# Kernel tuning notes

Hardware: AMD Instinct MI355X
Metric: run time of the kernel (lower is better)

The kernel has to match this reference:

```python
import jax, jax.numpy as jnp
import numpy as np

B = 65536          # batch (number of states)
M = 32             # obstacles per state -> x width = 2*M
PHI = [4, 64, 64, 64]
RHO = [64, 64, 64, 32]


def _init_mlp(key, dims, prefix):
    params = {}
    ks = jax.random.split(key, len(dims) - 1)
    for i, (din, dout) in enumerate(zip(dims[:-1], dims[1:])):
        scale = 1.0 / np.sqrt(din)
        params[f"{prefix}_W{i+1}"] = scale * jax.random.normal(ks[i], (din, dout), dtype=jnp.float32)
        params[f"{prefix}_b{i+1}"] = jnp.zeros((dout,), dtype=jnp.float32)
    return params


def setup_inputs() -> dict:
    key = jax.random.key(0)
    kx, kv, kphi, krho = jax.random.split(key, 4)
    inp = {
        "x": jax.random.normal(kx, (B, 2 * M), dtype=jnp.float32),
        "vel": jax.random.normal(kv, (B, 2), dtype=jnp.float32),
    }
    inp.update(_init_mlp(kphi, PHI, "phi"))
    inp.update(_init_mlp(krho, RHO, "rho"))
    return inp


def _mlp3(h, W1, b1, W2, b2, W3, b3):
    # FeedForward: activation between hidden layers, linear output
    h = jax.nn.relu(h @ W1 + b1)
    h = jax.nn.relu(h @ W2 + b2)
    return h @ W3 + b3


def reference(x, vel,
              phi_W1, phi_b1, phi_W2, phi_b2, phi_W3, phi_b3,
              rho_W1, rho_b1, rho_W2, rho_b2, rho_W3, rho_b3):
    b = x.shape[0]
    m = x.shape[1] // 2
    obs = x.reshape(b, m, 2)                                   # [B, M, 2]
    velb = jnp.broadcast_to(vel[:, None, :], (b, m, 2))        # [B, M, 2]
    inp = jnp.concatenate([obs, velb], axis=-1)                # [B, M, 4]
    # phi batched across all obstacle elements (replaces the per-i loop)
    h = _mlp3(inp, phi_W1, phi_b1, phi_W2, phi_b2, phi_W3, phi_b3)  # [B, M, 64]
    X = h.sum(axis=1)                                          # DeepSets sum pool -> [B, 64]
    return _mlp3(X, rho_W1, rho_b1, rho_W2, rho_b2, rho_W3, rho_b3)  # [B, 32]
```

## Files before the change

kernel.cpp:

```cpp
#include <hip/hip_runtime.h>

typedef _Float16 h16x8 __attribute__((ext_vector_type(8)));
typedef _Float16 h16x4 __attribute__((ext_vector_type(4)));
typedef _Float16 h16x2 __attribute__((ext_vector_type(2)));
typedef float    fx4   __attribute__((ext_vector_type(4)));

static __device__ __forceinline__ fx4 mfma16(h16x8 a, h16x8 b, fx4 c) {
  return __builtin_amdgcn_mfma_f32_16x16x32_f16(a, b, c, 0, 0, 0);
}

static __device__ __forceinline__ h16x2 splat2(float v) {
  const _Float16 h = (_Float16)v;
  h16x2 r; r[0] = h; r[1] = h; return r;
}

union ABfrag { h16x2 p[4]; h16x8 v; };


__global__ __launch_bounds__(256, 2)
void deepset_kernel(const float* __restrict__ x,   const float* __restrict__ vel,
                    const float* __restrict__ pW1, const float* __restrict__ pb1,
                    const float* __restrict__ pW2, const float* __restrict__ pb2,
                    const float* __restrict__ pW3, const float* __restrict__ pb3,
                    const float* __restrict__ rW1, const float* __restrict__ rb1,
                    const float* __restrict__ rW2, const float* __restrict__ rb2,
                    const float* __restrict__ rW3, const float* __restrict__ rb3,
                    float* __restrict__ out)
{
  __shared__ __align__(16) _Float16 h2T[4][16][72];
  __shared__ __align__(16) _Float16 Xlds[4][16][72];

  const int tid  = threadIdx.x;
  const int wave = tid >> 6;
  const int lane = tid & 63;
  const int q    = lane >> 4;
  const int c    = lane & 15;

  h16x2 wx[2][4], wy[2][4], wvx[2][4], wvy[2][4], bbp[2][4];
#pragma unroll
  for (int ks = 0; ks < 2; ++ks)
#pragma unroll
    for (int t = 0; t < 4; ++t) {
      const int f0 = 32*ks + 8*q + 2*t;
#pragma unroll
      for (int e = 0; e < 2; ++e) {
        wx [ks][t][e] = (_Float16)pW1[      f0 + e];
        wy [ks][t][e] = (_Float16)pW1[ 64 + f0 + e];
        wvx[ks][t][e] = (_Float16)pW1[128 + f0 + e];
        wvy[ks][t][e] = (_Float16)pW1[192 + f0 + e];
        bbp[ks][t][e] = (_Float16)pb1[      f0 + e];
      }
    }

  h16x8 B2[4][2];
#pragma unroll
  for (int ct = 0; ct < 4; ++ct)
#pragma unroll
    for (int ks = 0; ks < 2; ++ks) {
      h16x8 f2;
#pragma unroll
      for (int j = 0; j < 8; ++j)
        f2[j] = (_Float16)pW2[(32*ks + 8*q + j)*64 + 16*ct + c];
      B2[ct][ks] = f2;
    }
  float b2v[4];
#pragma unroll
  for (int ct = 0; ct < 4; ++ct) b2v[ct] = pb2[16*ct + c];

  const int sBaseBlock = blockIdx.x * 64;
  const int sBase = sBaseBlock + wave * 16;
  const h16x2 z2 = splat2(0.f);

  float4 xo_cur = ((const float4*)x)[(size_t)sBase*16 + c];
  float2 v_cur  = *(const float2*)(vel + 2*(size_t)sBase);

#pragma unroll 1
  for (int si = 0; si < 16; ++si) {
    float4 xo_nxt;
    float2 v_nxt;
    if (si < 15) {
      xo_nxt = ((const float4*)x)[(size_t)(sBase + si + 1)*16 + c];
      v_nxt  = *(const float2*)(vel + 2*(size_t)(sBase + si + 1));
    }
    const h16x2 vxp = splat2(v_cur.x);
    const h16x2 vyp = splat2(v_cur.y);
    h16x2 vbp[2][4];
#pragma unroll
    for (int ks = 0; ks < 2; ++ks)
#pragma unroll
      for (int t = 0; t < 4; ++t)
        vbp[ks][t] = vxp * wvx[ks][t] + vyp * wvy[ks][t] + bbp[ks][t];

    float Xacc[4] = {0.f, 0.f, 0.f, 0.f};
#pragma unroll
    for (int hh = 0; hh < 2; ++hh) {
      const h16x2 oxp = splat2(hh ? xo_cur.z : xo_cur.x);
      const h16x2 oyp = splat2(hh ? xo_cur.w : xo_cur.y);
      h16x8 A1[2];
#pragma unroll
      for (int ks = 0; ks < 2; ++ks) {
        ABfrag a;
#pragma unroll
        for (int t = 0; t < 4; ++t) {
          const h16x2 h = oxp * wx[ks][t] + oyp * wy[ks][t] + vbp[ks][t];
          a.p[t] = __builtin_elementwise_max(h, z2);
        }
        A1[ks] = a.v;
      }
#pragma unroll
      for (int ct = 0; ct < 4; ++ct) {
        fx4 acc = {0.f, 0.f, 0.f, 0.f};
        acc = mfma16(A1[0], B2[ct][0], acc);
        acc = mfma16(A1[1], B2[ct][1], acc);
#pragma unroll
        for (int r = 0; r < 4; ++r)
          Xacc[ct] += fmaxf(acc[r] + b2v[ct], 0.f);
      }
    }
#pragma unroll
    for (int ct = 0; ct < 4; ++ct) {
      float v = Xacc[ct];
      v += __shfl_down(v, 16);
      v += __shfl_down(v, 32);
      if (lane < 16) Xlds[wave][si][16*ct + c] = (_Float16)v;
    }
    xo_cur = xo_nxt;
    v_cur  = v_nxt;
  }

  __builtin_amdgcn_s_waitcnt(0xC07F);
  __builtin_amdgcn_wave_barrier();

  h16x8 B3[4][2];
#pragma unroll
  for (int ct = 0; ct < 4; ++ct)
#pragma unroll
    for (int ks = 0; ks < 2; ++ks) {
      h16x8 f3;
#pragma unroll
      for (int j = 0; j < 8; ++j)
        f3[j] = (_Float16)pW3[(32*ks + 8*q + j)*64 + 16*ct + c];
      B3[ct][ks] = f3;
    }
  float b3s[4];
#pragma unroll
  for (int ct = 0; ct < 4; ++ct) b3s[ct] = 32.f * pb3[16*ct + c];

  h16x8 AX[2];
#pragma unroll
  for (int ks = 0; ks < 2; ++ks)
    AX[ks] = *(const h16x8*)&Xlds[wave][c][32*ks + 8*q];

  fx4 C3[4];
#pragma unroll
  for (int ct = 0; ct < 4; ++ct) {
    fx4 acc = {0.f,0.f,0.f,0.f};
    acc = mfma16(AX[0], B3[ct][0], acc);
    acc = mfma16(AX[1], B3[ct][1], acc);
    C3[ct] = acc;
  }
#pragma unroll
  for (int r = 0; r < 4; ++r) {
    h16x4 pk;
#pragma unroll
    for (int ct = 0; ct < 4; ++ct)
      pk[ct] = (_Float16)(C3[ct][r] + b3s[ct]);
    *(h16x4*)&h2T[wave][4*q + r][4*c] = pk;
  }

  h16x8 R1[4][2], R2[4][2], R3[2][2];
#pragma unroll
  for (int ct = 0; ct < 4; ++ct)
#pragma unroll
    for (int ks = 0; ks < 2; ++ks) {
      h16x8 f1, f2;
#pragma unroll
      for (int j = 0; j < 8; ++j) {
        const int p = 32*ks + 8*q + j;
        const int f = 16*(p & 3) + (p >> 2);
        f1[j] = (_Float16)rW1[f*64 + 16*ct + c];
        f2[j] = (_Float16)rW2[f*64 + 16*ct + c];
      }
      R1[ct][ks] = f1;
      R2[ct][ks] = f2;
    }
#pragma unroll
  for (int ct = 0; ct < 2; ++ct)
#pragma unroll
    for (int ks = 0; ks < 2; ++ks) {
      h16x8 f3;
#pragma unroll
      for (int j = 0; j < 8; ++j) {
        const int p = 32*ks + 8*q + j;
        const int f = 16*(p & 3) + (p >> 2);
        f3[j] = (_Float16)rW3[f*32 + 16*ct + c];
      }
      R3[ct][ks] = f3;
    }
  float rb1v[4], rb2v[4], rb3v[2];
#pragma unroll
  for (int ct = 0; ct < 4; ++ct) { rb1v[ct] = rb1[16*ct + c]; rb2v[ct] = rb2[16*ct + c]; }
#pragma unroll
  for (int ct = 0; ct < 2; ++ct) rb3v[ct] = rb3[16*ct + c];

  __builtin_amdgcn_s_waitcnt(0xC07F);
  __builtin_amdgcn_wave_barrier();
  h16x8 A1r[2];
#pragma unroll
  for (int ks = 0; ks < 2; ++ks)
    A1r[ks] = *(const h16x8*)&h2T[wave][c][32*ks + 8*q];
  __builtin_amdgcn_wave_barrier();

  fx4 D1[4];
#pragma unroll
  for (int ct = 0; ct < 4; ++ct) {
    fx4 acc = {0.f,0.f,0.f,0.f};
    acc = mfma16(A1r[0], R1[ct][0], acc);
    acc = mfma16(A1r[1], R1[ct][1], acc);
    D1[ct] = acc;
  }
#pragma unroll
  for (int r = 0; r < 4; ++r) {
    h16x4 pk;
#pragma unroll
    for (int ct = 0; ct < 4; ++ct)
      pk[ct] = (_Float16)fmaxf(D1[ct][r] + rb1v[ct], 0.f);
    *(h16x4*)&h2T[wave][4*q + r][4*c] = pk;
  }
  __builtin_amdgcn_s_waitcnt(0xC07F);
  __builtin_amdgcn_wave_barrier();
  h16x8 A2r[2];
#pragma unroll
  for (int ks = 0; ks < 2; ++ks)
    A2r[ks] = *(const h16x8*)&h2T[wave][c][32*ks + 8*q];
  __builtin_amdgcn_wave_barrier();

  fx4 D2[4];
#pragma unroll
  for (int ct = 0; ct < 4; ++ct) {
    fx4 acc = {0.f,0.f,0.f,0.f};
    acc = mfma16(A2r[0], R2[ct][0], acc);
    acc = mfma16(A2r[1], R2[ct][1], acc);
    D2[ct] = acc;
  }
#pragma unroll
  for (int r = 0; r < 4; ++r) {
    h16x4 pk;
#pragma unroll
    for (int ct = 0; ct < 4; ++ct)
      pk[ct] = (_Float16)fmaxf(D2[ct][r] + rb2v[ct], 0.f);
    *(h16x4*)&h2T[wave][4*q + r][4*c] = pk;
  }
  __builtin_amdgcn_s_waitcnt(0xC07F);
  __builtin_amdgcn_wave_barrier();
  h16x8 A3r[2];
#pragma unroll
  for (int ks = 0; ks < 2; ++ks)
    A3r[ks] = *(const h16x8*)&h2T[wave][c][32*ks + 8*q];
  __builtin_amdgcn_wave_barrier();

  fx4 D3[2];
#pragma unroll
  for (int ct = 0; ct < 2; ++ct) {
    fx4 acc = {0.f,0.f,0.f,0.f};
    acc = mfma16(A3r[0], R3[ct][0], acc);
    acc = mfma16(A3r[1], R3[ct][1], acc);
    D3[ct] = acc;
  }
  const int srow = sBaseBlock + 16*wave + 4*q;
#pragma unroll
  for (int ct = 0; ct < 2; ++ct)
#pragma unroll
    for (int r = 0; r < 4; ++r)
      out[(size_t)(srow + r)*32 + 16*ct + c] = D3[ct][r] + rb3v[ct];
}

extern "C" void kernel_launch(void* const* d_in, const int* in_sizes, int n_in,
                              void* d_out, int out_size, void* d_ws, size_t ws_size,
                              hipStream_t stream) {
  const float* x   = (const float*)d_in[0];
  const float* vel = (const float*)d_in[1];
  const float* pW1 = (const float*)d_in[2];
  const float* pb1 = (const float*)d_in[3];
  const float* pW2 = (const float*)d_in[4];
  const float* pb2 = (const float*)d_in[5];
  const float* pW3 = (const float*)d_in[6];
  const float* pb3 = (const float*)d_in[7];
  const float* rW1 = (const float*)d_in[8];
  const float* rb1 = (const float*)d_in[9];
  const float* rW2 = (const float*)d_in[10];
  const float* rb2 = (const float*)d_in[11];
  const float* rW3 = (const float*)d_in[12];
  const float* rb3 = (const float*)d_in[13];
  float* out = (float*)d_out;

  const int B = in_sizes[0] / 64;
  deepset_kernel<<<dim3(B / 64), dim3(256), 0, stream>>>(
      x, vel, pW1, pb1, pW2, pb2, pW3, pb3,
      rW1, rb1, rW2, rb2, rW3, rb3, out);
}
```

Before: 136.0 us.

## Prepack fp16 weight fragments in a prep kernel and use single-wave blocks of 8 states

```diff
diff --git a/kernel.cpp b/kernel.cpp
--- a/kernel.cpp
+++ b/kernel.cpp
@@ -8,77 +8,105 @@
 static __device__ __forceinline__ fx4 mfma16(h16x8 a, h16x8 b, fx4 c) {
   return __builtin_amdgcn_mfma_f32_16x16x32_f16(a, b, c, 0, 0, 0);
 }
-
 static __device__ __forceinline__ h16x2 splat2(float v) {
-  const _Float16 h = (_Float16)v;
-  h16x2 r; r[0] = h; r[1] = h; return r;
-}
-
+  const _Float16 h = (_Float16)v; h16x2 r; r[0] = h; r[1] = h; return r;
+}
 union ABfrag { h16x2 p[4]; h16x8 v; };
 
 
-__global__ __launch_bounds__(256, 2)
-void deepset_kernel(const float* __restrict__ x,   const float* __restrict__ vel,
-                    const float* __restrict__ pW1, const float* __restrict__ pb1,
-                    const float* __restrict__ pW2, const float* __restrict__ pb2,
-                    const float* __restrict__ pW3, const float* __restrict__ pb3,
-                    const float* __restrict__ rW1, const float* __restrict__ rb1,
-                    const float* __restrict__ rW2, const float* __restrict__ rb2,
-                    const float* __restrict__ rW3, const float* __restrict__ rb3,
-                    float* __restrict__ out)
+__global__ __launch_bounds__(64)
+void prep_weights(const float* __restrict__ pW1, const float* __restrict__ pb1,
+                  const float* __restrict__ pW2, const float* __restrict__ pb2,
+                  const float* __restrict__ pW3, const float* __restrict__ pb3,
+                  const float* __restrict__ rW1, const float* __restrict__ rb1,
+                  const float* __restrict__ rW2, const float* __restrict__ rb2,
+                  const float* __restrict__ rW3, const float* __restrict__ rb3,
+                  _Float16* __restrict__ ws)
 {
-  __shared__ __align__(16) _Float16 h2T[4][16][72];
-  __shared__ __align__(16) _Float16 Xlds[4][16][72];
-
-  const int tid  = threadIdx.x;
-  const int wave = tid >> 6;
-  const int lane = tid & 63;
+  const int lane = threadIdx.x;
+  const int q = lane >> 4, c = lane & 15;
+  _Float16* W = ws + (size_t)lane * 512;
+
+#pragma unroll
+  for (int ct = 0; ct < 4; ++ct)
+#pragma unroll
+    for (int ks = 0; ks < 2; ++ks)
+#pragma unroll
+      for (int j = 0; j < 8; ++j) {
+        const int p = 32*ks + 8*q + j;
+        const int f = 16*(p & 3) + (p >> 2);
+        W[      (ct*2 + ks)*8 + j] = (_Float16)pW2[p*64 + 16*ct + c];
+        W[ 64 + (ct*2 + ks)*8 + j] = (_Float16)pW3[p*64 + 16*ct + c];
+        W[128 + (ct*2 + ks)*8 + j] = (_Float16)rW1[f*64 + 16*ct + c];
+        W[192 + (ct*2 + ks)*8 + j] = (_Float16)rW2[f*64 + 16*ct + c];
+        if (ct < 2)
+          W[256 + (ct*2 + ks)*8 + j] = (_Float16)rW3[f*32 + 16*ct + c];
+      }
+#pragma unroll
+  for (int ks = 0; ks < 2; ++ks)
+#pragma unroll
+    for (int i = 0; i < 8; ++i) {
+      const int f = 32*ks + 8*q + i;
+      W[288 + ks*8 + i] = (_Float16)pW1[      f];
+      W[304 + ks*8 + i] = (_Float16)pW1[ 64 + f];
+      W[320 + ks*8 + i] = (_Float16)pW1[128 + f];
+      W[336 + ks*8 + i] = (_Float16)pW1[192 + f];
+      W[352 + ks*8 + i] = (_Float16)pb1[      f];
+    }
+  float* F = (float*)(ws + (size_t)lane * 512) + 184;
+#pragma unroll
+  for (int ct = 0; ct < 4; ++ct) {
+    F[     ct] = pb2[16*ct + c];
+    F[ 4 + ct] = 32.f * pb3[16*ct + c];
+    F[ 8 + ct] = rb1[16*ct + c];
+    F[12 + ct] = rb2[16*ct + c];
+  }
+#pragma unroll
+  for (int ct = 0; ct < 2; ++ct) F[16 + ct] = rb3[16*ct + c];
+}
+
+__global__ __launch_bounds__(64, 5)
+void deepset_main(const float* __restrict__ x, const float* __restrict__ vel,
+                  const _Float16* __restrict__ ws, float* __restrict__ out)
+{
+  __shared__ __align__(16) _Float16 h2T[16][72];
+  __shared__ __align__(16) _Float16 Xlds[16][72];
+
+  const int lane = threadIdx.x & 63;
   const int q    = lane >> 4;
   const int c    = lane & 15;
 
-  h16x2 wx[2][4], wy[2][4], wvx[2][4], wvy[2][4], bbp[2][4];
-#pragma unroll
-  for (int ks = 0; ks < 2; ++ks)
-#pragma unroll
-    for (int t = 0; t < 4; ++t) {
-      const int f0 = 32*ks + 8*q + 2*t;
-#pragma unroll
-      for (int e = 0; e < 2; ++e) {
-        wx [ks][t][e] = (_Float16)pW1[      f0 + e];
-        wy [ks][t][e] = (_Float16)pW1[ 64 + f0 + e];
-        wvx[ks][t][e] = (_Float16)pW1[128 + f0 + e];
-        wvy[ks][t][e] = (_Float16)pW1[192 + f0 + e];
-        bbp[ks][t][e] = (_Float16)pb1[      f0 + e];
-      }
-    }
+  const h16x8* V = (const h16x8*)(ws + (size_t)lane * 512);
+  const float* F = (const float*)(ws + (size_t)lane * 512) + 184;
 
   h16x8 B2[4][2];
 #pragma unroll
   for (int ct = 0; ct < 4; ++ct)
 #pragma unroll
-    for (int ks = 0; ks < 2; ++ks) {
-      h16x8 f2;
-#pragma unroll
-      for (int j = 0; j < 8; ++j)
-        f2[j] = (_Float16)pW2[(32*ks + 8*q + j)*64 + 16*ct + c];
-      B2[ct][ks] = f2;
-    }
+    for (int ks = 0; ks < 2; ++ks) B2[ct][ks] = V[ct*2 + ks];
+  ABfrag wx[2], wy[2], wvx[2], wvy[2], bbp[2];
+#pragma unroll
+  for (int ks = 0; ks < 2; ++ks) {
+    wx [ks].v = V[36 + ks];
+    wy [ks].v = V[38 + ks];
+    wvx[ks].v = V[40 + ks];
+    wvy[ks].v = V[42 + ks];
+    bbp[ks].v = V[44 + ks];
+  }
   float b2v[4];
 #pragma unroll
-  for (int ct = 0; ct < 4; ++ct) b2v[ct] = pb2[16*ct + c];
-
-  const int sBaseBlock = blockIdx.x * 64;
-  const int sBase = sBaseBlock + wave * 16;
+  for (int ct = 0; ct < 4; ++ct) b2v[ct] = F[ct];
+
+  const int sBase = blockIdx.x * 8;
   const h16x2 z2 = splat2(0.f);
 
   float4 xo_cur = ((const float4*)x)[(size_t)sBase*16 + c];
   float2 v_cur  = *(const float2*)(vel + 2*(size_t)sBase);
 
 #pragma unroll 1
-  for (int si = 0; si < 16; ++si) {
-    float4 xo_nxt;
-    float2 v_nxt;
-    if (si < 15) {
+  for (int si = 0; si < 8; ++si) {
+    float4 xo_nxt; float2 v_nxt;
+    if (si < 7) {
       xo_nxt = ((const float4*)x)[(size_t)(sBase + si + 1)*16 + c];
       v_nxt  = *(const float2*)(vel + 2*(size_t)(sBase + si + 1));
     }
@@ -89,7 +117,7 @@
     for (int ks = 0; ks < 2; ++ks)
 #pragma unroll
       for (int t = 0; t < 4; ++t)
-        vbp[ks][t] = vxp * wvx[ks][t] + vyp * wvy[ks][t] + bbp[ks][t];
+        vbp[ks][t] = vxp * wvx[ks].p[t] + vyp * wvy[ks].p[t] + bbp[ks].p[t];
 
     float Xacc[4] = {0.f, 0.f, 0.f, 0.f};
 #pragma unroll
@@ -102,7 +130,7 @@
         ABfrag a;
 #pragma unroll
         for (int t = 0; t < 4; ++t) {
-          const h16x2 h = oxp * wx[ks][t] + oyp * wy[ks][t] + vbp[ks][t];
+          const h16x2 h = oxp * wx[ks].p[t] + oyp * wy[ks].p[t] + vbp[ks][t];
           a.p[t] = __builtin_elementwise_max(h, z2);
         }
         A1[ks] = a.v;
@@ -122,7 +150,7 @@
       float v = Xacc[ct];
       v += __shfl_down(v, 16);
       v += __shfl_down(v, 32);
-      if (lane < 16) Xlds[wave][si][16*ct + c] = (_Float16)v;
+      if (lane < 16) Xlds[si][16*ct + c] = (_Float16)v;
     }
     xo_cur = xo_nxt;
     v_cur  = v_nxt;
@@ -131,25 +159,33 @@
   __builtin_amdgcn_s_waitcnt(0xC07F);
   __builtin_amdgcn_wave_barrier();
 
-  h16x8 B3[4][2];
+  h16x8 B3[4][2], R1[4][2], R2[4][2], R3[2][2];
 #pragma unroll
   for (int ct = 0; ct < 4; ++ct)
 #pragma unroll
     for (int ks = 0; ks < 2; ++ks) {
-      h16x8 f3;
-#pragma unroll
-      for (int j = 0; j < 8; ++j)
-        f3[j] = (_Float16)pW3[(32*ks + 8*q + j)*64 + 16*ct + c];
-      B3[ct][ks] = f3;
-    }
-  float b3s[4];
-#pragma unroll
-  for (int ct = 0; ct < 4; ++ct) b3s[ct] = 32.f * pb3[16*ct + c];
+      B3[ct][ks] = V[ 8 + ct*2 + ks];
+      R1[ct][ks] = V[16 + ct*2 + ks];
+      R2[ct][ks] = V[24 + ct*2 + ks];
+    }
+#pragma unroll
+  for (int ct = 0; ct < 2; ++ct)
+#pragma unroll
+    for (int ks = 0; ks < 2; ++ks) R3[ct][ks] = V[32 + ct*2 + ks];
+  float b3s[4], rb1v[4], rb2v[4], rb3v[2];
+#pragma unroll
+  for (int ct = 0; ct < 4; ++ct) {
+    b3s[ct]  = F[ 4 + ct];
+    rb1v[ct] = F[ 8 + ct];
+    rb2v[ct] = F[12 + ct];
+  }
+#pragma unroll
+  for (int ct = 0; ct < 2; ++ct) rb3v[ct] = F[16 + ct];
 
   h16x8 AX[2];
 #pragma unroll
   for (int ks = 0; ks < 2; ++ks)
-    AX[ks] = *(const h16x8*)&Xlds[wave][c][32*ks + 8*q];
+    AX[ks] = *(const h16x8*)&Xlds[c][32*ks + 8*q];
 
   fx4 C3[4];
 #pragma unroll
@@ -165,50 +201,14 @@
 #pragma unroll
     for (int ct = 0; ct < 4; ++ct)
       pk[ct] = (_Float16)(C3[ct][r] + b3s[ct]);
-    *(h16x4*)&h2T[wave][4*q + r][4*c] = pk;
-  }
-
-  h16x8 R1[4][2], R2[4][2], R3[2][2];
-#pragma unroll
-  for (int ct = 0; ct < 4; ++ct)
-#pragma unroll
-    for (int ks = 0; ks < 2; ++ks) {
-      h16x8 f1, f2;
-#pragma unroll
-      for (int j = 0; j < 8; ++j) {
-        const int p = 32*ks + 8*q + j;
-        const int f = 16*(p & 3) + (p >> 2);
-        f1[j] = (_Float16)rW1[f*64 + 16*ct + c];
-        f2[j] = (_Float16)rW2[f*64 + 16*ct + c];
-      }
-      R1[ct][ks] = f1;
-      R2[ct][ks] = f2;
-    }
-#pragma unroll
-  for (int ct = 0; ct < 2; ++ct)
-#pragma unroll
-    for (int ks = 0; ks < 2; ++ks) {
-      h16x8 f3;
-#pragma unroll
-      for (int j = 0; j < 8; ++j) {
-        const int p = 32*ks + 8*q + j;
-        const int f = 16*(p & 3) + (p >> 2);
-        f3[j] = (_Float16)rW3[f*32 + 16*ct + c];
-      }
-      R3[ct][ks] = f3;
-    }
-  float rb1v[4], rb2v[4], rb3v[2];
-#pragma unroll
-  for (int ct = 0; ct < 4; ++ct) { rb1v[ct] = rb1[16*ct + c]; rb2v[ct] = rb2[16*ct + c]; }
-#pragma unroll
-  for (int ct = 0; ct < 2; ++ct) rb3v[ct] = rb3[16*ct + c];
-
+    *(h16x4*)&h2T[4*q + r][4*c] = pk;
+  }
   __builtin_amdgcn_s_waitcnt(0xC07F);
   __builtin_amdgcn_wave_barrier();
   h16x8 A1r[2];
 #pragma unroll
   for (int ks = 0; ks < 2; ++ks)
-    A1r[ks] = *(const h16x8*)&h2T[wave][c][32*ks + 8*q];
+    A1r[ks] = *(const h16x8*)&h2T[c][32*ks + 8*q];
   __builtin_amdgcn_wave_barrier();
 
   fx4 D1[4];
@@ -225,14 +225,14 @@
 #pragma unroll
     for (int ct = 0; ct < 4; ++ct)
       pk[ct] = (_Float16)fmaxf(D1[ct][r] + rb1v[ct], 0.f);
-    *(h16x4*)&h2T[wave][4*q + r][4*c] = pk;
+    *(h16x4*)&h2T[4*q + r][4*c] = pk;
   }
   __builtin_amdgcn_s_waitcnt(0xC07F);
   __builtin_amdgcn_wave_barrier();
   h16x8 A2r[2];
 #pragma unroll
   for (int ks = 0; ks < 2; ++ks)
-    A2r[ks] = *(const h16x8*)&h2T[wave][c][32*ks + 8*q];
+    A2r[ks] = *(const h16x8*)&h2T[c][32*ks + 8*q];
   __builtin_amdgcn_wave_barrier();
 
   fx4 D2[4];
@@ -249,14 +249,14 @@
 #pragma unroll
     for (int ct = 0; ct < 4; ++ct)
       pk[ct] = (_Float16)fmaxf(D2[ct][r] + rb2v[ct], 0.f);
-    *(h16x4*)&h2T[wave][4*q + r][4*c] = pk;
+    *(h16x4*)&h2T[4*q + r][4*c] = pk;
   }
   __builtin_amdgcn_s_waitcnt(0xC07F);
   __builtin_amdgcn_wave_barrier();
   h16x8 A3r[2];
 #pragma unroll
   for (int ks = 0; ks < 2; ++ks)
-    A3r[ks] = *(const h16x8*)&h2T[wave][c][32*ks + 8*q];
+    A3r[ks] = *(const h16x8*)&h2T[c][32*ks + 8*q];
   __builtin_amdgcn_wave_barrier();
 
   fx4 D3[2];
@@ -267,12 +267,14 @@
     acc = mfma16(A3r[1], R3[ct][1], acc);
     D3[ct] = acc;
   }
-  const int srow = sBaseBlock + 16*wave + 4*q;
-#pragma unroll
-  for (int ct = 0; ct < 2; ++ct)
-#pragma unroll
-    for (int r = 0; r < 4; ++r)
-      out[(size_t)(srow + r)*32 + 16*ct + c] = D3[ct][r] + rb3v[ct];
+  if (q < 2) {
+    const int srow = sBase + 4*q;
+#pragma unroll
+    for (int ct = 0; ct < 2; ++ct)
+#pragma unroll
+      for (int r = 0; r < 4; ++r)
+        out[(size_t)(srow + r)*32 + 16*ct + c] = D3[ct][r] + rb3v[ct];
+  }
 }
 
 extern "C" void kernel_launch(void* const* d_in, const int* in_sizes, int n_in,
@@ -293,9 +295,11 @@
   const float* rW3 = (const float*)d_in[12];
   const float* rb3 = (const float*)d_in[13];
   float* out = (float*)d_out;
+  _Float16* ws = (_Float16*)d_ws;
+
+  prep_weights<<<dim3(1), dim3(64), 0, stream>>>(
+      pW1, pb1, pW2, pb2, pW3, pb3, rW1, rb1, rW2, rb2, rW3, rb3, ws);
 
   const int B = in_sizes[0] / 64;
-  deepset_kernel<<<dim3(B / 64), dim3(256), 0, stream>>>(
-      x, vel, pW1, pb1, pW2, pb2, pW3, pb3,
-      rW1, rb1, rW2, rb2, rW3, rb3, out);
-}
+  deepset_main<<<dim3(B / 8), dim3(64), 0, stream>>>(x, vel, ws, out);
+}
```

New measurement: 288.7 us. +112.3%, slower.

## Remap phi MFMA rows to states and stage x tile in LDS

Applied to the files above, without the earlier changes.

```diff
diff --git a/kernel.cpp b/kernel.cpp
--- a/kernel.cpp
+++ b/kernel.cpp
@@ -8,35 +8,41 @@
 static __device__ __forceinline__ fx4 mfma16(h16x8 a, h16x8 b, fx4 c) {
   return __builtin_amdgcn_mfma_f32_16x16x32_f16(a, b, c, 0, 0, 0);
 }
-
 static __device__ __forceinline__ h16x2 splat2(float v) {
-  const _Float16 h = (_Float16)v;
-  h16x2 r; r[0] = h; r[1] = h; return r;
-}
-
+  const _Float16 h = (_Float16)v; h16x2 r; r[0] = h; r[1] = h; return r;
+}
 union ABfrag { h16x2 p[4]; h16x8 v; };
 
 
-__global__ __launch_bounds__(256, 2)
-void deepset_kernel(const float* __restrict__ x,   const float* __restrict__ vel,
-                    const float* __restrict__ pW1, const float* __restrict__ pb1,
-                    const float* __restrict__ pW2, const float* __restrict__ pb2,
-                    const float* __restrict__ pW3, const float* __restrict__ pb3,
-                    const float* __restrict__ rW1, const float* __restrict__ rb1,
-                    const float* __restrict__ rW2, const float* __restrict__ rb2,
-                    const float* __restrict__ rW3, const float* __restrict__ rb3,
-                    float* __restrict__ out)
+__global__ __launch_bounds__(64, 4)
+void deepset_main(const float* __restrict__ x,   const float* __restrict__ vel,
+                  const float* __restrict__ pW1, const float* __restrict__ pb1,
+                  const float* __restrict__ pW2, const float* __restrict__ pb2,
+                  const float* __restrict__ pW3, const float* __restrict__ pb3,
+                  const float* __restrict__ rW1, const float* __restrict__ rb1,
+                  const float* __restrict__ rW2, const float* __restrict__ rb2,
+                  const float* __restrict__ rW3, const float* __restrict__ rb3,
+                  float* __restrict__ out)
 {
-  __shared__ __align__(16) _Float16 h2T[4][16][72];
-  __shared__ __align__(16) _Float16 Xlds[4][16][72];
-
-  const int tid  = threadIdx.x;
-  const int wave = tid >> 6;
-  const int lane = tid & 63;
+  __shared__ __align__(16) float    xT[16][68];
+  __shared__ __align__(16) _Float16 h2T[16][72];
+
+  const int lane = threadIdx.x & 63;
   const int q    = lane >> 4;
   const int c    = lane & 15;
-
-  h16x2 wx[2][4], wy[2][4], wvx[2][4], wvy[2][4], bbp[2][4];
+  const int sBase = blockIdx.x * 16;
+
+  {
+    const int s0 = lane >> 2, ch = lane & 3;
+#pragma unroll
+    for (int k = 0; k < 4; ++k) {
+      const float4 g = ((const float4*)x)[(size_t)(sBase + s0)*16 + ch + 4*k];
+      *(float4*)&xT[s0][(ch + 4*k)*4] = g;
+    }
+  }
+  const float2 vc = *(const float2*)(vel + 2*(size_t)(sBase + c));
+
+  h16x2 wx[2][4], wy[2][4], vbp[2][4];
 #pragma unroll
   for (int ks = 0; ks < 2; ++ks)
 #pragma unroll
@@ -44,11 +50,10 @@
       const int f0 = 32*ks + 8*q + 2*t;
 #pragma unroll
       for (int e = 0; e < 2; ++e) {
-        wx [ks][t][e] = (_Float16)pW1[      f0 + e];
-        wy [ks][t][e] = (_Float16)pW1[ 64 + f0 + e];
-        wvx[ks][t][e] = (_Float16)pW1[128 + f0 + e];
-        wvy[ks][t][e] = (_Float16)pW1[192 + f0 + e];
-        bbp[ks][t][e] = (_Float16)pb1[      f0 + e];
+        wx[ks][t][e] = (_Float16)pW1[      f0 + e];
+        wy[ks][t][e] = (_Float16)pW1[ 64 + f0 + e];
+        vbp[ks][t][e] = (_Float16)fmaf(vc.x, pW1[128 + f0 + e],
+                                  fmaf(vc.y, pW1[192 + f0 + e], pb1[f0 + e]));
       }
     }
 
@@ -67,122 +72,60 @@
 #pragma unroll
   for (int ct = 0; ct < 4; ++ct) b2v[ct] = pb2[16*ct + c];
 
-  const int sBaseBlock = blockIdx.x * 64;
-  const int sBase = sBaseBlock + wave * 16;
+  __builtin_amdgcn_s_waitcnt(0xC07F);
+  __builtin_amdgcn_wave_barrier();
+
   const h16x2 z2 = splat2(0.f);
-
-  float4 xo_cur = ((const float4*)x)[(size_t)sBase*16 + c];
-  float2 v_cur  = *(const float2*)(vel + 2*(size_t)sBase);
-
+  float Xacc[4][4] = {};
+
+  float4 p_cur = *(const float4*)&xT[c][0];
 #pragma unroll 1
-  for (int si = 0; si < 16; ++si) {
-    float4 xo_nxt;
-    float2 v_nxt;
-    if (si < 15) {
-      xo_nxt = ((const float4*)x)[(size_t)(sBase + si + 1)*16 + c];
-      v_nxt  = *(const float2*)(vel + 2*(size_t)(sBase + si + 1));
-    }
-    const h16x2 vxp = splat2(v_cur.x);
-    const h16x2 vyp = splat2(v_cur.y);
-    h16x2 vbp[2][4];
-#pragma unroll
-    for (int ks = 0; ks < 2; ++ks)
-#pragma unroll
-      for (int t = 0; t < 4; ++t)
-        vbp[ks][t] = vxp * wvx[ks][t] + vyp * wvy[ks][t] + bbp[ks][t];
-
-    float Xacc[4] = {0.f, 0.f, 0.f, 0.f};
+  for (int oo = 0; oo < 16; ++oo) {
+    float4 p_nxt;
+    if (oo < 15) p_nxt = *(const float4*)&xT[c][4*(oo + 1)];
 #pragma unroll
     for (int hh = 0; hh < 2; ++hh) {
-      const h16x2 oxp = splat2(hh ? xo_cur.z : xo_cur.x);
-      const h16x2 oyp = splat2(hh ? xo_cur.w : xo_cur.y);
+      const h16x2 ox = splat2(hh ? p_cur.z : p_cur.x);
+      const h16x2 oy = splat2(hh ? p_cur.w : p_cur.y);
       h16x8 A1[2];
 #pragma unroll
       for (int ks = 0; ks < 2; ++ks) {
         ABfrag a;
 #pragma unroll
         for (int t = 0; t < 4; ++t) {
-          const h16x2 h = oxp * wx[ks][t] + oyp * wy[ks][t] + vbp[ks][t];
+          const h16x2 h = ox * wx[ks][t] + oy * wy[ks][t] + vbp[ks][t];
           a.p[t] = __builtin_elementwise_max(h, z2);
         }
         A1[ks] = a.v;
       }
 #pragma unroll
       for (int ct = 0; ct < 4; ++ct) {
-        fx4 acc = {0.f, 0.f, 0.f, 0.f};
+        fx4 acc = {b2v[ct], b2v[ct], b2v[ct], b2v[ct]};
         acc = mfma16(A1[0], B2[ct][0], acc);
         acc = mfma16(A1[1], B2[ct][1], acc);
 #pragma unroll
         for (int r = 0; r < 4; ++r)
-          Xacc[ct] += fmaxf(acc[r] + b2v[ct], 0.f);
-      }
-    }
-#pragma unroll
-    for (int ct = 0; ct < 4; ++ct) {
-      float v = Xacc[ct];
-      v += __shfl_down(v, 16);
-      v += __shfl_down(v, 32);
-      if (lane < 16) Xlds[wave][si][16*ct + c] = (_Float16)v;
-    }
-    xo_cur = xo_nxt;
-    v_cur  = v_nxt;
-  }
-
-  __builtin_amdgcn_s_waitcnt(0xC07F);
-  __builtin_amdgcn_wave_barrier();
-
-  h16x8 B3[4][2];
+          Xacc[ct][r] += fmaxf(acc[r], 0.f);
+      }
+    }
+    p_cur = p_nxt;
+  }
+
+  h16x8 B3[4][2], R1[4][2], R2[4][2], R3[2][2];
 #pragma unroll
   for (int ct = 0; ct < 4; ++ct)
 #pragma unroll
     for (int ks = 0; ks < 2; ++ks) {
-      h16x8 f3;
-#pragma unroll
-      for (int j = 0; j < 8; ++j)
-        f3[j] = (_Float16)pW3[(32*ks + 8*q + j)*64 + 16*ct + c];
-      B3[ct][ks] = f3;
-    }
-  float b3s[4];
-#pragma unroll
-  for (int ct = 0; ct < 4; ++ct) b3s[ct] = 32.f * pb3[16*ct + c];
-
-  h16x8 AX[2];
-#pragma unroll
-  for (int ks = 0; ks < 2; ++ks)
-    AX[ks] = *(const h16x8*)&Xlds[wave][c][32*ks + 8*q];
-
-  fx4 C3[4];
-#pragma unroll
-  for (int ct = 0; ct < 4; ++ct) {
-    fx4 acc = {0.f,0.f,0.f,0.f};
-    acc = mfma16(AX[0], B3[ct][0], acc);
-    acc = mfma16(AX[1], B3[ct][1], acc);
-    C3[ct] = acc;
-  }
-#pragma unroll
-  for (int r = 0; r < 4; ++r) {
-    h16x4 pk;
-#pragma unroll
-    for (int ct = 0; ct < 4; ++ct)
-      pk[ct] = (_Float16)(C3[ct][r] + b3s[ct]);
-    *(h16x4*)&h2T[wave][4*q + r][4*c] = pk;
-  }
-
-  h16x8 R1[4][2], R2[4][2], R3[2][2];
-#pragma unroll
-  for (int ct = 0; ct < 4; ++ct)
-#pragma unroll
-    for (int ks = 0; ks < 2; ++ks) {
-      h16x8 f1, f2;
+      h16x8 f3, f1, f2;
 #pragma unroll
       for (int j = 0; j < 8; ++j) {
         const int p = 32*ks + 8*q + j;
         const int f = 16*(p & 3) + (p >> 2);
+        f3[j] = (_Float16)pW3[f*64 + 16*ct + c];
         f1[j] = (_Float16)rW1[f*64 + 16*ct + c];
         f2[j] = (_Float16)rW2[f*64 + 16*ct + c];
       }
-      R1[ct][ks] = f1;
-      R2[ct][ks] = f2;
+      B3[ct][ks] = f3; R1[ct][ks] = f1; R2[ct][ks] = f2;
     }
 #pragma unroll
   for (int ct = 0; ct < 2; ++ct)
@@ -197,24 +140,58 @@
       }
       R3[ct][ks] = f3;
     }
-  float rb1v[4], rb2v[4], rb3v[2];
-#pragma unroll
-  for (int ct = 0; ct < 4; ++ct) { rb1v[ct] = rb1[16*ct + c]; rb2v[ct] = rb2[16*ct + c]; }
+  float b3s[4], rb1v[4], rb2v[4], rb3v[2];
+#pragma unroll
+  for (int ct = 0; ct < 4; ++ct) {
+    b3s[ct]  = 32.f * pb3[16*ct + c];
+    rb1v[ct] = rb1[16*ct + c];
+    rb2v[ct] = rb2[16*ct + c];
+  }
 #pragma unroll
   for (int ct = 0; ct < 2; ++ct) rb3v[ct] = rb3[16*ct + c];
 
+#pragma unroll
+  for (int r = 0; r < 4; ++r) {
+    h16x4 pk;
+#pragma unroll
+    for (int ct = 0; ct < 4; ++ct) pk[ct] = (_Float16)Xacc[ct][r];
+    *(h16x4*)&h2T[4*q + r][4*c] = pk;
+  }
+  __builtin_amdgcn_s_waitcnt(0xC07F);
+  __builtin_amdgcn_wave_barrier();
+  h16x8 AX[2];
+#pragma unroll
+  for (int ks = 0; ks < 2; ++ks)
+    AX[ks] = *(const h16x8*)&h2T[c][32*ks + 8*q];
+  __builtin_amdgcn_wave_barrier();
+
+  fx4 C3[4];
+#pragma unroll
+  for (int ct = 0; ct < 4; ++ct) {
+    fx4 acc = {b3s[ct], b3s[ct], b3s[ct], b3s[ct]};
+    acc = mfma16(AX[0], B3[ct][0], acc);
+    acc = mfma16(AX[1], B3[ct][1], acc);
+    C3[ct] = acc;
+  }
+#pragma unroll
+  for (int r = 0; r < 4; ++r) {
+    h16x4 pk;
+#pragma unroll
+    for (int ct = 0; ct < 4; ++ct) pk[ct] = (_Float16)C3[ct][r];
+    *(h16x4*)&h2T[4*q + r][4*c] = pk;
+  }
   __builtin_amdgcn_s_waitcnt(0xC07F);
   __builtin_amdgcn_wave_barrier();
   h16x8 A1r[2];
 #pragma unroll
   for (int ks = 0; ks < 2; ++ks)
-    A1r[ks] = *(const h16x8*)&h2T[wave][c][32*ks + 8*q];
+    A1r[ks] = *(const h16x8*)&h2T[c][32*ks + 8*q];
   __builtin_amdgcn_wave_barrier();
 
   fx4 D1[4];
 #pragma unroll
   for (int ct = 0; ct < 4; ++ct) {
-    fx4 acc = {0.f,0.f,0.f,0.f};
+    fx4 acc = {rb1v[ct], rb1v[ct], rb1v[ct], rb1v[ct]};
     acc = mfma16(A1r[0], R1[ct][0], acc);
     acc = mfma16(A1r[1], R1[ct][1], acc);
     D1[ct] = acc;
@@ -224,21 +201,21 @@
     h16x4 pk;
 #pragma unroll
     for (int ct = 0; ct < 4; ++ct)
-      pk[ct] = (_Float16)fmaxf(D1[ct][r] + rb1v[ct], 0.f);
-    *(h16x4*)&h2T[wave][4*q + r][4*c] = pk;
+      pk[ct] = (_Float16)fmaxf(D1[ct][r], 0.f);
+    *(h16x4*)&h2T[4*q + r][4*c] = pk;
   }
   __builtin_amdgcn_s_waitcnt(0xC07F);
   __builtin_amdgcn_wave_barrier();
   h16x8 A2r[2];
 #pragma unroll
   for (int ks = 0; ks < 2; ++ks)
-    A2r[ks] = *(const h16x8*)&h2T[wave][c][32*ks + 8*q];
+    A2r[ks] = *(const h16x8*)&h2T[c][32*ks + 8*q];
   __builtin_amdgcn_wave_barrier();
 
   fx4 D2[4];
 #pragma unroll
   for (int ct = 0; ct < 4; ++ct) {
-    fx4 acc = {0.f,0.f,0.f,0.f};
+    fx4 acc = {rb2v[ct], rb2v[ct], rb2v[ct], rb2v[ct]};
     acc = mfma16(A2r[0], R2[ct][0], acc);
     acc = mfma16(A2r[1], R2[ct][1], acc);
     D2[ct] = acc;
@@ -248,31 +225,31 @@
     h16x4 pk;
 #pragma unroll
     for (int ct = 0; ct < 4; ++ct)
-      pk[ct] = (_Float16)fmaxf(D2[ct][r] + rb2v[ct], 0.f);
-    *(h16x4*)&h2T[wave][4*q + r][4*c] = pk;
+      pk[ct] = (_Float16)fmaxf(D2[ct][r], 0.f);
+    *(h16x4*)&h2T[4*q + r][4*c] = pk;
   }
   __builtin_amdgcn_s_waitcnt(0xC07F);
   __builtin_amdgcn_wave_barrier();
   h16x8 A3r[2];
 #pragma unroll
   for (int ks = 0; ks < 2; ++ks)
-    A3r[ks] = *(const h16x8*)&h2T[wave][c][32*ks + 8*q];
+    A3r[ks] = *(const h16x8*)&h2T[c][32*ks + 8*q];
   __builtin_amdgcn_wave_barrier();
 
   fx4 D3[2];
 #pragma unroll
   for (int ct = 0; ct < 2; ++ct) {
-    fx4 acc = {0.f,0.f,0.f,0.f};
+    fx4 acc = {rb3v[ct], rb3v[ct], rb3v[ct], rb3v[ct]};
     acc = mfma16(A3r[0], R3[ct][0], acc);
     acc = mfma16(A3r[1], R3[ct][1], acc);
     D3[ct] = acc;
   }
-  const int srow = sBaseBlock + 16*wave + 4*q;
+  const int srow = sBase + 4*q;
 #pragma unroll
   for (int ct = 0; ct < 2; ++ct)
 #pragma unroll
     for (int r = 0; r < 4; ++r)
-      out[(size_t)(srow + r)*32 + 16*ct + c] = D3[ct][r] + rb3v[ct];
+      out[(size_t)(srow + r)*32 + 16*ct + c] = D3[ct][r];
 }
 
 extern "C" void kernel_launch(void* const* d_in, const int* in_sizes, int n_in,
@@ -295,7 +272,7 @@
   float* out = (float*)d_out;
 
   const int B = in_sizes[0] / 64;
-  deepset_kernel<<<dim3(B / 64), dim3(256), 0, stream>>>(
+  deepset_main<<<dim3(B / 16), dim3(64), 0, stream>>>(
       x, vel, pW1, pb1, pW2, pb2, pW3, pb3,
       rW1, rb1, rW2, rb2, rW3, rb3, out);
 }
```

Measured after the change: 134.0 us. Within noise of the previous version (-1.5%).
